# Kernel optimization log

Measured on AMD Instinct MI355X. Metric: run time of the kernel, lower is better.

Reference implementation:

```python
import jax, jax.numpy as jnp
import numpy as np

NUM_HEADS = 8

def setup_inputs() -> dict:
    key = jax.random.key(0)
    k1, k2, k3, k4, k5 = jax.random.split(key, 5)
    B, N, C = 4, 2048, 512
    x = jax.random.normal(k1, (B, N, C), dtype=jnp.float32)
    s = 1.0 / np.sqrt(C)
    qkv_w = jax.random.uniform(k2, (3 * C, C), dtype=jnp.float32, minval=-s, maxval=s)
    qkv_b = jax.random.uniform(k3, (3 * C,), dtype=jnp.float32, minval=-s, maxval=s)
    proj_w = jax.random.uniform(k4, (C, C), dtype=jnp.float32, minval=-s, maxval=s)
    proj_b = jax.random.uniform(k5, (C,), dtype=jnp.float32, minval=-s, maxval=s)
    return {"x": x, "qkv_w": qkv_w, "qkv_b": qkv_b, "proj_w": proj_w, "proj_b": proj_b}

def reference(x, qkv_w, qkv_b, proj_w, proj_b):
    B, N, C = x.shape
    H = NUM_HEADS
    D = C // H
    scale = D ** -0.5
    # qkv: [B,N,3C] -> [3,B,H,N,D]
    qkv = (jnp.einsum('bnc,oc->bno', x, qkv_w) + qkv_b)
    qkv = qkv.reshape(B, N, 3, H, D).transpose(2, 0, 3, 1, 4)
    q, k, v = qkv[0], qkv[1], qkv[2]
    attn = jnp.einsum('bhnd,bhmd->bhnm', q, k) * scale  # [B,H,N,N]
    attn = jax.nn.softmax(attn, axis=-1)
    out = jnp.einsum('bhnm,bhmd->bhnd', attn, v)  # [B,H,N,D]
    out = out.transpose(0, 2, 1, 3).reshape(B, N, C)
    return jnp.einsum('bnc,oc->bno', out, proj_w) + proj_b
```

## Files before the change

kernel.cpp:

```cpp
#include <hip/hip_runtime.h>
#include <stdint.h>


typedef short bf16x8 __attribute__((ext_vector_type(8)));
typedef float f32x2  __attribute__((ext_vector_type(2)));
typedef float f32x4  __attribute__((ext_vector_type(4)));
typedef float f32x16 __attribute__((ext_vector_type(16)));
typedef unsigned int u32x4 __attribute__((ext_vector_type(4)));

__device__ __forceinline__ unsigned short f2bf(float f) {
    unsigned int u = __builtin_bit_cast(unsigned int, f);
    u += 0x7fffu + ((u >> 16) & 1u);
    return (unsigned short)(u >> 16);
}
__device__ __forceinline__ unsigned int pk2(float a, float b) {
    return (unsigned int)f2bf(a) | ((unsigned int)f2bf(b) << 16);
}
__device__ __forceinline__ float fexp2(float x) {
    return __builtin_amdgcn_exp2f(x);
}
__device__ __forceinline__ bf16x8 ld8_f32(const float* __restrict__ p) {
    float4 f0 = *(const float4*)p;
    float4 f1 = *(const float4*)(p + 4);
    u32x4 u = {pk2(f0.x, f0.y), pk2(f0.z, f0.w), pk2(f1.x, f1.y), pk2(f1.z, f1.w)};
    return __builtin_bit_cast(bf16x8, u);
}
__device__ __forceinline__ void async16(const void* g, void* l) {
    __builtin_amdgcn_global_load_lds(
        (const __attribute__((address_space(1))) unsigned int*)g,
        (__attribute__((address_space(3))) unsigned int*)l,
        16, 0, 0);
}

#define MFMA16(a, b, c) __builtin_amdgcn_mfma_f32_16x16x32_bf16((a), (b), (c), 0, 0, 0)
#define MFMA32(a, b, c) __builtin_amdgcn_mfma_f32_32x32x16_bf16((a), (b), (c), 0, 0, 0)

__global__ void cvt_bf16(const float* __restrict__ x,
                         const float* __restrict__ w,
                         const float* __restrict__ w2,
                         unsigned short* __restrict__ xb,
                         unsigned short* __restrict__ wb,
                         unsigned short* __restrict__ wb2)
{
    const int G = 524288 + 98304 + 32768;
    for (int idx = blockIdx.x * 256 + threadIdx.x; idx < G; idx += gridDim.x * 256) {
        if (idx < 524288)
            *(bf16x8*)(xb + (size_t)idx * 8) = ld8_f32(x + (size_t)idx * 8);
        else if (idx < 524288 + 98304) {
            int j = idx - 524288;
            *(bf16x8*)(wb + (size_t)j * 8) = ld8_f32(w + (size_t)j * 8);
        } else {
            int j = idx - 524288 - 98304;
            *(bf16x8*)(wb2 + (size_t)j * 8) = ld8_f32(w2 + (size_t)j * 8);
        }
    }
}

__global__ __launch_bounds__(256, 4)
void gemm_qkv(const unsigned short* __restrict__ A,
              const unsigned short* __restrict__ B,
              const float* __restrict__ bias,
              unsigned short* __restrict__ out0,
              unsigned short* __restrict__ out1,
              unsigned short* __restrict__ out2,
              int K)
{
    __shared__ unsigned short sA[128 * 32];
    __shared__ unsigned short sB[128 * 32];

    const int tid  = threadIdx.x;
    const int wave = tid >> 6, lane = tid & 63;
    const int l = lane & 15, q16 = lane >> 4;
    const int wm = wave >> 1, wn = wave & 1;
    const int bid = blockIdx.x;
    const int slot = bid >> 3;
    const int m0 = ((bid & 7) * 8 + slot / 12) * 128;
    const int n0 = (slot % 12) * 128;

    f32x4 acc[4][4];
#pragma unroll
    for (int i = 0; i < 4; ++i)
#pragma unroll
        for (int j = 0; j < 4; ++j)
            acc[i][j] = (f32x4){0.f, 0.f, 0.f, 0.f};

    for (int k0 = 0; k0 < K; k0 += 32) {
#pragma unroll
        for (int call = 0; call < 2; ++call) {
            int L = call * 256 + tid;
            int r = L >> 2, c = L & 3;
            async16(A + (size_t)(m0 + r) * K + k0 + c * 8, sA + L * 8);
            async16(B + (size_t)(n0 + r) * K + k0 + c * 8, sB + L * 8);
        }
        __syncthreads();

        bf16x8 af[4], bfr[4];
#pragma unroll
        for (int i = 0; i < 4; ++i)
            af[i] = *(const bf16x8*)(sA + ((wm * 64 + i * 16 + l) * 4 + q16) * 8);
#pragma unroll
        for (int j = 0; j < 4; ++j)
            bfr[j] = *(const bf16x8*)(sB + ((wn * 64 + j * 16 + l) * 4 + q16) * 8);
#pragma unroll
        for (int i = 0; i < 4; ++i)
#pragma unroll
            for (int j = 0; j < 4; ++j)
                acc[i][j] = MFMA16(af[i], bfr[j], acc[i][j]);
        __syncthreads();
    }

    const float lscale = 0.18033688f;
#pragma unroll
    for (int i = 0; i < 4; ++i) {
#pragma unroll
        for (int j = 0; j < 4; ++j) {
            int col = n0 + wn * 64 + j * 16 + l;
            float bv = bias[col];
#pragma unroll
            for (int r = 0; r < 4; ++r) {
                int row = m0 + wm * 64 + i * 16 + q16 * 4 + r;
                float val = acc[i][j][r] + bv;
                int which = col >> 9;
                int h = (col >> 6) & 7, d = col & 63;
                int b = row >> 11, n = row & 2047;
                if (which == 0)
                    out0[(size_t)(((b * 8 + h) * 2048) + n) * 64 + d] = f2bf(val * lscale);
                else if (which == 1)
                    out1[(size_t)(((b * 8 + h) * 2048) + n) * 64 + d] = f2bf(val);
                else {
                    int np = (n & ~12) | ((n & 8) >> 1) | ((n & 4) << 1);
                    out2[(size_t)(((b * 8 + h) * 64) + d) * 2048 + np] = f2bf(val);
                }
            }
        }
    }
}

__global__ __launch_bounds__(256, 4)
void gemm_out(const unsigned short* __restrict__ A,
              const unsigned short* __restrict__ B,
              const float* __restrict__ bias,
              float* __restrict__ outf,
              int K, int N)
{
    __shared__ unsigned short sA[64 * 32];
    __shared__ unsigned short sB[128 * 32];

    const int tid  = threadIdx.x;
    const int wave = tid >> 6, lane = tid & 63;
    const int l = lane & 15, q16 = lane >> 4;
    const int wm = wave >> 1, wn = wave & 1;
    const int bid = blockIdx.x;
    const int slot = bid >> 3;
    const int m0 = ((bid & 7) * 16 + (slot >> 2)) * 64;
    const int n0 = (slot & 3) * 128;

    f32x4 acc[2][4];
#pragma unroll
    for (int i = 0; i < 2; ++i)
#pragma unroll
        for (int j = 0; j < 4; ++j)
            acc[i][j] = (f32x4){0.f, 0.f, 0.f, 0.f};

    for (int k0 = 0; k0 < K; k0 += 32) {
        {
            int r = tid >> 2, c = tid & 3;
            async16(A + (size_t)(m0 + r) * K + k0 + c * 8, sA + tid * 8);
        }
#pragma unroll
        for (int call = 0; call < 2; ++call) {
            int L = call * 256 + tid;
            int r = L >> 2, c = L & 3;
            async16(B + (size_t)(n0 + r) * K + k0 + c * 8, sB + L * 8);
        }
        __syncthreads();

        bf16x8 af[2], bfr[4];
#pragma unroll
        for (int i = 0; i < 2; ++i)
            af[i] = *(const bf16x8*)(sA + ((wm * 32 + i * 16 + l) * 4 + q16) * 8);
#pragma unroll
        for (int j = 0; j < 4; ++j)
            bfr[j] = *(const bf16x8*)(sB + ((wn * 64 + j * 16 + l) * 4 + q16) * 8);
#pragma unroll
        for (int i = 0; i < 2; ++i)
#pragma unroll
            for (int j = 0; j < 4; ++j)
                acc[i][j] = MFMA16(af[i], bfr[j], acc[i][j]);
        __syncthreads();
    }

#pragma unroll
    for (int i = 0; i < 2; ++i) {
#pragma unroll
        for (int j = 0; j < 4; ++j) {
            int col = n0 + wn * 64 + j * 16 + l;
            float bv = bias[col];
#pragma unroll
            for (int r = 0; r < 4; ++r) {
                int row = m0 + wm * 32 + i * 16 + q16 * 4 + r;
                outf[(size_t)row * N + col] = acc[i][j][r] + bv;
            }
        }
    }
}

__global__ __launch_bounds__(256, 2)
void attn_fused(const unsigned short* __restrict__ Q,
                const unsigned short* __restrict__ Km,
                const unsigned short* __restrict__ Vt,
                unsigned short* __restrict__ O)
{
    __shared__ unsigned short sK[2][128 * 64];
    __shared__ unsigned short sVt[2][64 * 128];

    const int tid  = threadIdx.x;
    const int wave = tid >> 6, lane = tid & 63;
    const int l31 = lane & 31, h = lane >> 5;
    const int swz = l31 & 7;
    const int bid = blockIdx.x;
    const int slot = bid >> 3;
    const int bh = (bid & 7) * 4 + (slot >> 4);
    const int n0 = (slot & 15) * 128;
    const int q0 = n0 + wave * 32;

    const unsigned short* Kp = Km + (size_t)bh * 2048 * 64;
    const unsigned short* Vp = Vt + (size_t)bh * 64 * 2048;
    const unsigned short* sKf = &sK[0][0];
    const unsigned short* sVf = &sVt[0][0];

    int ka[4], va[2][2];
#pragma unroll
    for (int ks = 0; ks < 4; ++ks)
        ka[ks] = l31 * 64 + ((ks * 2 + h) ^ swz) * 8;
#pragma unroll
    for (int m1 = 0; m1 < 2; ++m1)
#pragma unroll
        for (int ks2 = 0; ks2 < 2; ++ks2)
            va[m1][ks2] = l31 * 128 + ((m1 * 4 + ks2 * 2 + h) ^ swz) * 8;

    int ksrc[4], vsrc[4], dst[4];
#pragma unroll
    for (int c = 0; c < 4; ++c) {
        int s = wave * 256 + c * 64 + lane;
        int rk = s >> 3;
        ksrc[c] = rk * 64 + ((s & 7) ^ (rk & 7)) * 8;
        int rv = s >> 4;
        vsrc[c] = rv * 2048 + ((s & 15) ^ (rv & 7)) * 8;
        dst[c] = s * 8;
    }

    bf16x8 qf[4];
#pragma unroll
    for (int ks = 0; ks < 4; ++ks)
        qf[ks] = *(const bf16x8*)(Q + (size_t)(bh * 2048 + q0 + l31) * 64 + ks * 16 + h * 8);

    f32x16 oacc[2];
#pragma unroll
    for (int dt = 0; dt < 2; ++dt)
#pragma unroll
        for (int e = 0; e < 16; ++e) oacc[dt][e] = 0.f;
    f32x16 Zv;
#pragma unroll
    for (int e = 0; e < 16; ++e) Zv[e] = 0.f;
    f32x2 l2 = {0.f, 0.f};

#pragma unroll
    for (int c = 0; c < 4; ++c) {
        async16(Kp + ksrc[c], (void*)(sKf + dst[c]));
        async16(Vp + vsrc[c], (void*)(sVf + dst[c]));
    }
    __syncthreads();

    for (int it = 0; it < 16; ++it) {
        const int nb = ((it + 1) & 1) * 8192;
        if (it < 15) {
            int kv = (it + 1) * 128;
#pragma unroll
            for (int c = 0; c < 4; ++c)
                async16(Kp + (size_t)kv * 64 + ksrc[c], (void*)(sKf + nb + dst[c]));
        }

        f32x16 sacc[4];
#pragma unroll
        for (int mt = 0; mt < 4; ++mt) {
            bf16x8 kf0 = *(const bf16x8*)(sKf + ka[0] + mt * 2048);
            sacc[mt] = MFMA32(kf0, qf[0], Zv);
#pragma unroll
            for (int ks = 1; ks < 4; ++ks) {
                bf16x8 kf = *(const bf16x8*)(sKf + ka[ks] + mt * 2048);
                sacc[mt] = MFMA32(kf, qf[ks], sacc[mt]);
            }
        }

        if (it < 15) {
            int kv = (it + 1) * 128;
#pragma unroll
            for (int c = 0; c < 4; ++c)
                async16(Vp + (size_t)kv + vsrc[c], (void*)(sVf + nb + dst[c]));
        }

        unsigned int pk[4][4][2];
#pragma unroll
        for (int mt = 0; mt < 4; ++mt)
#pragma unroll
            for (int g = 0; g < 4; ++g) {
                float p0 = fexp2(sacc[mt][4 * g + 0]);
                float p1 = fexp2(sacc[mt][4 * g + 1]);
                float p2 = fexp2(sacc[mt][4 * g + 2]);
                float p3 = fexp2(sacc[mt][4 * g + 3]);
                l2 += (f32x2){p0, p1};
                l2 += (f32x2){p2, p3};
                pk[mt][g][0] = __builtin_amdgcn_perm(
                    __builtin_bit_cast(unsigned int, p1),
                    __builtin_bit_cast(unsigned int, p0), 0x07060302u);
                pk[mt][g][1] = __builtin_amdgcn_perm(
                    __builtin_bit_cast(unsigned int, p3),
                    __builtin_bit_cast(unsigned int, p2), 0x07060302u);
            }

#pragma unroll
        for (int mt = 0; mt < 4; ++mt) {
#pragma unroll
            for (int ks2 = 0; ks2 < 2; ++ks2) {
                u32x4 bu;
                bu[0] = pk[mt][2 * ks2][0];
                bu[1] = pk[mt][2 * ks2][1];
                bu[2] = pk[mt][2 * ks2 + 1][0];
                bu[3] = pk[mt][2 * ks2 + 1][1];
                bf16x8 bfrag = __builtin_bit_cast(bf16x8, bu);
#pragma unroll
                for (int dt = 0; dt < 2; ++dt) {
                    bf16x8 vf = *(const bf16x8*)(sVf + va[mt & 1][ks2]
                                                 + (mt >> 1) * 64 + dt * 4096);
                    oacc[dt] = MFMA32(vf, bfrag, oacc[dt]);
                }
            }
        }

#pragma unroll
        for (int ks = 0; ks < 4; ++ks) ka[ks] ^= 8192;
        va[0][0] ^= 8192; va[0][1] ^= 8192; va[1][0] ^= 8192; va[1][1] ^= 8192;
        __syncthreads();
    }

    float l_run = l2[0] + l2[1];
    l_run += __shfl_xor(l_run, 32);
    const int b = bh >> 3, hh = bh & 7;
    float inv = 1.f / fmaxf(l_run, 1e-20f);
    unsigned short* obase = O + ((size_t)(b * 2048 + q0 + l31)) * 512 + hh * 64;
#pragma unroll
    for (int dt = 0; dt < 2; ++dt)
#pragma unroll
        for (int g = 0; g < 4; ++g) {
            int d = dt * 32 + 8 * g + 4 * h;
            unsigned int w0 = pk2(oacc[dt][4 * g + 0] * inv, oacc[dt][4 * g + 1] * inv);
            unsigned int w1 = pk2(oacc[dt][4 * g + 2] * inv, oacc[dt][4 * g + 3] * inv);
            uint2 w = {w0, w1};
            *(uint2*)(obase + d) = w;
        }
}

extern "C" void kernel_launch(void* const* d_in, const int* in_sizes, int n_in,
                              void* d_out, int out_size, void* d_ws, size_t ws_size,
                              hipStream_t stream)
{
    const float* x      = (const float*)d_in[0];
    const float* qkv_w  = (const float*)d_in[1];
    const float* qkv_b  = (const float*)d_in[2];
    const float* proj_w = (const float*)d_in[3];
    const float* proj_b = (const float*)d_in[4];

    const size_t PER = 4u * 8u * 2048u * 64u;
    unsigned short* q_ws  = (unsigned short*)d_ws;
    unsigned short* k_ws  = q_ws  + PER;
    unsigned short* vt_ws = k_ws  + PER;
    unsigned short* ao_ws = vt_ws + PER;
    unsigned short* wb2   = ao_ws + PER;

    unsigned short* xb = (unsigned short*)d_out;
    unsigned short* wb = xb + PER;

    cvt_bf16<<<dim3(640), 256, 0, stream>>>(x, qkv_w, proj_w, xb, wb, wb2);
    gemm_qkv<<<dim3(768), 256, 0, stream>>>(xb, wb, qkv_b, q_ws, k_ws, vt_ws, 512);
    attn_fused<<<dim3(512), 256, 0, stream>>>(q_ws, k_ws, vt_ws, ao_ws);
    gemm_out<<<dim3(512), 256, 0, stream>>>(ao_ws, wb2, proj_b, (float*)d_out, 512, 512);
}
```

Before: 156.1 us.

## Process two query tiles per wave in attention, halving waves per block

The attention kernel now runs with 2 waves of 128 threads instead of 4, and each wave handles 64 query rows as two 32-row tiles. Each K and V fragment read from shared memory is reused across both tiles, cutting LDS reads per MFMA. Each thread issues twice as many async copies, and register pressure roughly doubles for the accumulators. Launch bounds drop to one block per SM, which lowers wave-level parallelism and may limit latency hiding.

```diff
diff --git a/kernel.cpp b/kernel.cpp
--- a/kernel.cpp
+++ b/kernel.cpp
@@ -205,7 +205,7 @@
     }
 }
 
-__global__ __launch_bounds__(256, 2)
+__global__ __launch_bounds__(128, 1)
 void attn_fused(const unsigned short* __restrict__ Q,
                 const unsigned short* __restrict__ Km,
                 const unsigned short* __restrict__ Vt,
@@ -222,7 +222,7 @@
     const int slot = bid >> 3;
     const int bh = (bid & 7) * 4 + (slot >> 4);
     const int n0 = (slot & 15) * 128;
-    const int q0 = n0 + wave * 32;
+    const int q0 = n0 + wave * 64;
 
     const unsigned short* Kp = Km + (size_t)bh * 2048 * 64;
     const unsigned short* Vp = Vt + (size_t)bh * 64 * 2048;
@@ -239,10 +239,10 @@
         for (int ks2 = 0; ks2 < 2; ++ks2)
             va[m1][ks2] = l31 * 128 + ((m1 * 4 + ks2 * 2 + h) ^ swz) * 8;
 
-    int ksrc[4], vsrc[4], dst[4];
-#pragma unroll
-    for (int c = 0; c < 4; ++c) {
-        int s = wave * 256 + c * 64 + lane;
+    int ksrc[8], vsrc[8], dst[8];
+#pragma unroll
+    for (int c = 0; c < 8; ++c) {
+        int s = c * 128 + tid;
         int rk = s >> 3;
         ksrc[c] = rk * 64 + ((s & 7) ^ (rk & 7)) * 8;
         int rv = s >> 4;
@@ -250,23 +250,30 @@
         dst[c] = s * 8;
     }
 
-    bf16x8 qf[4];
-#pragma unroll
-    for (int ks = 0; ks < 4; ++ks)
-        qf[ks] = *(const bf16x8*)(Q + (size_t)(bh * 2048 + q0 + l31) * 64 + ks * 16 + h * 8);
-
-    f32x16 oacc[2];
-#pragma unroll
-    for (int dt = 0; dt < 2; ++dt)
-#pragma unroll
-        for (int e = 0; e < 16; ++e) oacc[dt][e] = 0.f;
+    bf16x8 qf[2][4];
+#pragma unroll
+    for (int qt = 0; qt < 2; ++qt)
+#pragma unroll
+        for (int ks = 0; ks < 4; ++ks)
+            qf[qt][ks] = *(const bf16x8*)(Q + (size_t)(bh * 2048 + q0 + qt * 32 + l31) * 64
+                                          + ks * 16 + h * 8);
+
+    f32x16 oacc[2][2];
+#pragma unroll
+    for (int qt = 0; qt < 2; ++qt)
+#pragma unroll
+        for (int dt = 0; dt < 2; ++dt)
+#pragma unroll
+            for (int e = 0; e < 16; ++e) oacc[qt][dt][e] = 0.f;
     f32x16 Zv;
 #pragma unroll
     for (int e = 0; e < 16; ++e) Zv[e] = 0.f;
-    f32x2 l2 = {0.f, 0.f};
-
-#pragma unroll
-    for (int c = 0; c < 4; ++c) {
+    f32x2 l2[2];
+    l2[0] = (f32x2){0.f, 0.f};
+    l2[1] = (f32x2){0.f, 0.f};
+
+#pragma unroll
+    for (int c = 0; c < 8; ++c) {
         async16(Kp + ksrc[c], (void*)(sKf + dst[c]));
         async16(Vp + vsrc[c], (void*)(sVf + dst[c]));
     }
@@ -277,63 +284,71 @@
         if (it < 15) {
             int kv = (it + 1) * 128;
 #pragma unroll
-            for (int c = 0; c < 4; ++c)
+            for (int c = 0; c < 8; ++c)
                 async16(Kp + (size_t)kv * 64 + ksrc[c], (void*)(sKf + nb + dst[c]));
         }
 
-        f32x16 sacc[4];
+        f32x16 sacc[2][4];
 #pragma unroll
         for (int mt = 0; mt < 4; ++mt) {
             bf16x8 kf0 = *(const bf16x8*)(sKf + ka[0] + mt * 2048);
-            sacc[mt] = MFMA32(kf0, qf[0], Zv);
+            sacc[0][mt] = MFMA32(kf0, qf[0][0], Zv);
+            sacc[1][mt] = MFMA32(kf0, qf[1][0], Zv);
 #pragma unroll
             for (int ks = 1; ks < 4; ++ks) {
                 bf16x8 kf = *(const bf16x8*)(sKf + ka[ks] + mt * 2048);
-                sacc[mt] = MFMA32(kf, qf[ks], sacc[mt]);
+                sacc[0][mt] = MFMA32(kf, qf[0][ks], sacc[0][mt]);
+                sacc[1][mt] = MFMA32(kf, qf[1][ks], sacc[1][mt]);
             }
         }
 
         if (it < 15) {
             int kv = (it + 1) * 128;
 #pragma unroll
-            for (int c = 0; c < 4; ++c)
+            for (int c = 0; c < 8; ++c)
                 async16(Vp + (size_t)kv + vsrc[c], (void*)(sVf + nb + dst[c]));
         }
 
-        unsigned int pk[4][4][2];
-#pragma unroll
-        for (int mt = 0; mt < 4; ++mt)
-#pragma unroll
-            for (int g = 0; g < 4; ++g) {
-                float p0 = fexp2(sacc[mt][4 * g + 0]);
-                float p1 = fexp2(sacc[mt][4 * g + 1]);
-                float p2 = fexp2(sacc[mt][4 * g + 2]);
-                float p3 = fexp2(sacc[mt][4 * g + 3]);
-                l2 += (f32x2){p0, p1};
-                l2 += (f32x2){p2, p3};
-                pk[mt][g][0] = __builtin_amdgcn_perm(
-                    __builtin_bit_cast(unsigned int, p1),
-                    __builtin_bit_cast(unsigned int, p0), 0x07060302u);
-                pk[mt][g][1] = __builtin_amdgcn_perm(
-                    __builtin_bit_cast(unsigned int, p3),
-                    __builtin_bit_cast(unsigned int, p2), 0x07060302u);
-            }
-
 #pragma unroll
         for (int mt = 0; mt < 4; ++mt) {
+            unsigned int pk[2][4][2];
+#pragma unroll
+            for (int qt = 0; qt < 2; ++qt) {
+#pragma unroll
+                for (int g = 0; g < 4; ++g) {
+                    float p0 = fexp2(sacc[qt][mt][4 * g + 0]);
+                    float p1 = fexp2(sacc[qt][mt][4 * g + 1]);
+                    float p2 = fexp2(sacc[qt][mt][4 * g + 2]);
+                    float p3 = fexp2(sacc[qt][mt][4 * g + 3]);
+                    l2[qt] += (f32x2){p0, p1};
+                    l2[qt] += (f32x2){p2, p3};
+                    pk[qt][g][0] = __builtin_amdgcn_perm(
+                        __builtin_bit_cast(unsigned int, p1),
+                        __builtin_bit_cast(unsigned int, p0), 0x07060302u);
+                    pk[qt][g][1] = __builtin_amdgcn_perm(
+                        __builtin_bit_cast(unsigned int, p3),
+                        __builtin_bit_cast(unsigned int, p2), 0x07060302u);
+                }
+            }
 #pragma unroll
             for (int ks2 = 0; ks2 < 2; ++ks2) {
-                u32x4 bu;
-                bu[0] = pk[mt][2 * ks2][0];
-                bu[1] = pk[mt][2 * ks2][1];
-                bu[2] = pk[mt][2 * ks2 + 1][0];
-                bu[3] = pk[mt][2 * ks2 + 1][1];
-                bf16x8 bfrag = __builtin_bit_cast(bf16x8, bu);
+                u32x4 bu0, bu1;
+                bu0[0] = pk[0][2 * ks2][0];
+                bu0[1] = pk[0][2 * ks2][1];
+                bu0[2] = pk[0][2 * ks2 + 1][0];
+                bu0[3] = pk[0][2 * ks2 + 1][1];
+                bu1[0] = pk[1][2 * ks2][0];
+                bu1[1] = pk[1][2 * ks2][1];
+                bu1[2] = pk[1][2 * ks2 + 1][0];
+                bu1[3] = pk[1][2 * ks2 + 1][1];
+                bf16x8 bf0 = __builtin_bit_cast(bf16x8, bu0);
+                bf16x8 bf1 = __builtin_bit_cast(bf16x8, bu1);
 #pragma unroll
                 for (int dt = 0; dt < 2; ++dt) {
                     bf16x8 vf = *(const bf16x8*)(sVf + va[mt & 1][ks2]
                                                  + (mt >> 1) * 64 + dt * 4096);
-                    oacc[dt] = MFMA32(vf, bfrag, oacc[dt]);
+                    oacc[0][dt] = MFMA32(vf, bf0, oacc[0][dt]);
+                    oacc[1][dt] = MFMA32(vf, bf1, oacc[1][dt]);
                 }
             }
         }
@@ -344,21 +359,26 @@
         __syncthreads();
     }
 
-    float l_run = l2[0] + l2[1];
-    l_run += __shfl_xor(l_run, 32);
     const int b = bh >> 3, hh = bh & 7;
-    float inv = 1.f / fmaxf(l_run, 1e-20f);
-    unsigned short* obase = O + ((size_t)(b * 2048 + q0 + l31)) * 512 + hh * 64;
-#pragma unroll
-    for (int dt = 0; dt < 2; ++dt)
-#pragma unroll
-        for (int g = 0; g < 4; ++g) {
-            int d = dt * 32 + 8 * g + 4 * h;
-            unsigned int w0 = pk2(oacc[dt][4 * g + 0] * inv, oacc[dt][4 * g + 1] * inv);
-            unsigned int w1 = pk2(oacc[dt][4 * g + 2] * inv, oacc[dt][4 * g + 3] * inv);
-            uint2 w = {w0, w1};
-            *(uint2*)(obase + d) = w;
-        }
+#pragma unroll
+    for (int qt = 0; qt < 2; ++qt) {
+        float l_run = l2[qt][0] + l2[qt][1];
+        l_run += __shfl_xor(l_run, 32);
+        float inv = 1.f / fmaxf(l_run, 1e-20f);
+        unsigned short* obase = O + ((size_t)(b * 2048 + q0 + qt * 32 + l31)) * 512 + hh * 64;
+#pragma unroll
+        for (int dt = 0; dt < 2; ++dt)
+#pragma unroll
+            for (int g = 0; g < 4; ++g) {
+                int d = dt * 32 + 8 * g + 4 * h;
+                unsigned int w0 = pk2(oacc[qt][dt][4 * g + 0] * inv,
+                                      oacc[qt][dt][4 * g + 1] * inv);
+                unsigned int w1 = pk2(oacc[qt][dt][4 * g + 2] * inv,
+                                      oacc[qt][dt][4 * g + 3] * inv);
+                uint2 w = {w0, w1};
+                *(uint2*)(obase + d) = w;
+            }
+    }
 }
 
 extern "C" void kernel_launch(void* const* d_in, const int* in_sizes, int n_in,
@@ -383,6 +403,6 @@
 
     cvt_bf16<<<dim3(640), 256, 0, stream>>>(x, qkv_w, proj_w, xb, wb, wb2);
     gemm_qkv<<<dim3(768), 256, 0, stream>>>(xb, wb, qkv_b, q_ws, k_ws, vt_ws, 512);
-    attn_fused<<<dim3(512), 256, 0, stream>>>(q_ws, k_ws, vt_ws, ao_ws);
+    attn_fused<<<dim3(512), 128, 0, stream>>>(q_ws, k_ws, vt_ws, ao_ws);
     gemm_out<<<dim3(512), 256, 0, stream>>>(ao_ws, wb2, proj_b, (float*)d_out, 512, 512);
 }
```

After: 169.9 us. 1.09x slower.

## Split attention KV tiles across wave pairs and reduce partial outputs in LDS

Applied to the files above, without the earlier changes.

The attention kernel now runs 512 threads per block. Each pair of waves shares 32 query rows and splits every 128-wide KV tile, so each wave handles 64 keys. At the end, partial O accumulators and row sums from the second wave of each pair are added through shared memory before normalization. This halves per-wave MFMA work and register pressure (pk array shrinks) to raise occupancy and latency hiding. The cost is an extra LDS reduction with a block-wide sync and half the waves idle during the epilogue.

```diff
diff --git a/kernel.cpp b/kernel.cpp
--- a/kernel.cpp
+++ b/kernel.cpp
@@ -205,55 +205,56 @@
     }
 }
 
-__global__ __launch_bounds__(256, 2)
+__global__ __launch_bounds__(512, 4)
 void attn_fused(const unsigned short* __restrict__ Q,
                 const unsigned short* __restrict__ Km,
                 const unsigned short* __restrict__ Vt,
                 unsigned short* __restrict__ O)
 {
-    __shared__ unsigned short sK[2][128 * 64];
-    __shared__ unsigned short sVt[2][64 * 128];
+    __shared__ unsigned short sAll[32768];
 
     const int tid  = threadIdx.x;
     const int wave = tid >> 6, lane = tid & 63;
     const int l31 = lane & 31, h = lane >> 5;
     const int swz = l31 & 7;
+    const int qq = wave >> 1, kh = wave & 1;
     const int bid = blockIdx.x;
     const int slot = bid >> 3;
     const int bh = (bid & 7) * 4 + (slot >> 4);
     const int n0 = (slot & 15) * 128;
-    const int q0 = n0 + wave * 32;
+    const int q0 = n0 + qq * 32;
 
     const unsigned short* Kp = Km + (size_t)bh * 2048 * 64;
     const unsigned short* Vp = Vt + (size_t)bh * 64 * 2048;
-    const unsigned short* sKf = &sK[0][0];
-    const unsigned short* sVf = &sVt[0][0];
+    unsigned short* sKf = sAll;
+    unsigned short* sVf = sAll + 16384;
 
     int ka[4], va[2][2];
 #pragma unroll
     for (int ks = 0; ks < 4; ++ks)
-        ka[ks] = l31 * 64 + ((ks * 2 + h) ^ swz) * 8;
+        ka[ks] = (kh * 64 + l31) * 64 + ((ks * 2 + h) ^ swz) * 8;
 #pragma unroll
     for (int m1 = 0; m1 < 2; ++m1)
 #pragma unroll
         for (int ks2 = 0; ks2 < 2; ++ks2)
-            va[m1][ks2] = l31 * 128 + ((m1 * 4 + ks2 * 2 + h) ^ swz) * 8;
-
-    int ksrc[4], vsrc[4], dst[4];
-#pragma unroll
-    for (int c = 0; c < 4; ++c) {
-        int s = wave * 256 + c * 64 + lane;
+            va[m1][ks2] = l31 * 128 + ((m1 * 4 + ks2 * 2 + h) ^ swz) * 8 + kh * 64;
+
+    int ksrc[2], vsrc[2], dstv[2];
+#pragma unroll
+    for (int c = 0; c < 2; ++c) {
+        int s = c * 512 + tid;
         int rk = s >> 3;
         ksrc[c] = rk * 64 + ((s & 7) ^ (rk & 7)) * 8;
         int rv = s >> 4;
         vsrc[c] = rv * 2048 + ((s & 15) ^ (rv & 7)) * 8;
-        dst[c] = s * 8;
+        dstv[c] = s * 8;
     }
 
     bf16x8 qf[4];
 #pragma unroll
     for (int ks = 0; ks < 4; ++ks)
-        qf[ks] = *(const bf16x8*)(Q + (size_t)(bh * 2048 + q0 + l31) * 64 + ks * 16 + h * 8);
+        qf[ks] = *(const bf16x8*)(Q + (size_t)(bh * 2048 + q0 + l31) * 64
+                                  + ks * 16 + h * 8);
 
     f32x16 oacc[2];
 #pragma unroll
@@ -266,9 +267,9 @@
     f32x2 l2 = {0.f, 0.f};
 
 #pragma unroll
-    for (int c = 0; c < 4; ++c) {
-        async16(Kp + ksrc[c], (void*)(sKf + dst[c]));
-        async16(Vp + vsrc[c], (void*)(sVf + dst[c]));
+    for (int c = 0; c < 2; ++c) {
+        async16(Kp + ksrc[c], (void*)(sKf + dstv[c]));
+        async16(Vp + vsrc[c], (void*)(sVf + dstv[c]));
     }
     __syncthreads();
 
@@ -277,13 +278,13 @@
         if (it < 15) {
             int kv = (it + 1) * 128;
 #pragma unroll
-            for (int c = 0; c < 4; ++c)
-                async16(Kp + (size_t)kv * 64 + ksrc[c], (void*)(sKf + nb + dst[c]));
-        }
-
-        f32x16 sacc[4];
-#pragma unroll
-        for (int mt = 0; mt < 4; ++mt) {
+            for (int c = 0; c < 2; ++c)
+                async16(Kp + (size_t)kv * 64 + ksrc[c], (void*)(sKf + nb + dstv[c]));
+        }
+
+        f32x16 sacc[2];
+#pragma unroll
+        for (int mt = 0; mt < 2; ++mt) {
             bf16x8 kf0 = *(const bf16x8*)(sKf + ka[0] + mt * 2048);
             sacc[mt] = MFMA32(kf0, qf[0], Zv);
 #pragma unroll
@@ -296,13 +297,13 @@
         if (it < 15) {
             int kv = (it + 1) * 128;
 #pragma unroll
-            for (int c = 0; c < 4; ++c)
-                async16(Vp + (size_t)kv + vsrc[c], (void*)(sVf + nb + dst[c]));
-        }
-
-        unsigned int pk[4][4][2];
-#pragma unroll
-        for (int mt = 0; mt < 4; ++mt)
+            for (int c = 0; c < 2; ++c)
+                async16(Vp + (size_t)kv + vsrc[c], (void*)(sVf + nb + dstv[c]));
+        }
+
+#pragma unroll
+        for (int mt = 0; mt < 2; ++mt) {
+            unsigned int pk[4][2];
 #pragma unroll
             for (int g = 0; g < 4; ++g) {
                 float p0 = fexp2(sacc[mt][4 * g + 0]);
@@ -311,28 +312,24 @@
                 float p3 = fexp2(sacc[mt][4 * g + 3]);
                 l2 += (f32x2){p0, p1};
                 l2 += (f32x2){p2, p3};
-                pk[mt][g][0] = __builtin_amdgcn_perm(
+                pk[g][0] = __builtin_amdgcn_perm(
                     __builtin_bit_cast(unsigned int, p1),
                     __builtin_bit_cast(unsigned int, p0), 0x07060302u);
-                pk[mt][g][1] = __builtin_amdgcn_perm(
+                pk[g][1] = __builtin_amdgcn_perm(
                     __builtin_bit_cast(unsigned int, p3),
                     __builtin_bit_cast(unsigned int, p2), 0x07060302u);
             }
-
-#pragma unroll
-        for (int mt = 0; mt < 4; ++mt) {
 #pragma unroll
             for (int ks2 = 0; ks2 < 2; ++ks2) {
                 u32x4 bu;
-                bu[0] = pk[mt][2 * ks2][0];
-                bu[1] = pk[mt][2 * ks2][1];
-                bu[2] = pk[mt][2 * ks2 + 1][0];
-                bu[3] = pk[mt][2 * ks2 + 1][1];
+                bu[0] = pk[2 * ks2][0];
+                bu[1] = pk[2 * ks2][1];
+                bu[2] = pk[2 * ks2 + 1][0];
+                bu[3] = pk[2 * ks2 + 1][1];
                 bf16x8 bfrag = __builtin_bit_cast(bf16x8, bu);
 #pragma unroll
                 for (int dt = 0; dt < 2; ++dt) {
-                    bf16x8 vf = *(const bf16x8*)(sVf + va[mt & 1][ks2]
-                                                 + (mt >> 1) * 64 + dt * 4096);
+                    bf16x8 vf = *(const bf16x8*)(sVf + va[mt][ks2] + dt * 4096);
                     oacc[dt] = MFMA32(vf, bfrag, oacc[dt]);
                 }
             }
@@ -344,21 +341,47 @@
         __syncthreads();
     }
 
-    float l_run = l2[0] + l2[1];
-    l_run += __shfl_xor(l_run, 32);
-    const int b = bh >> 3, hh = bh & 7;
-    float inv = 1.f / fmaxf(l_run, 1e-20f);
-    unsigned short* obase = O + ((size_t)(b * 2048 + q0 + l31)) * 512 + hh * 64;
-#pragma unroll
-    for (int dt = 0; dt < 2; ++dt)
-#pragma unroll
-        for (int g = 0; g < 4; ++g) {
-            int d = dt * 32 + 8 * g + 4 * h;
-            unsigned int w0 = pk2(oacc[dt][4 * g + 0] * inv, oacc[dt][4 * g + 1] * inv);
-            unsigned int w1 = pk2(oacc[dt][4 * g + 2] * inv, oacc[dt][4 * g + 3] * inv);
-            uint2 w = {w0, w1};
-            *(uint2*)(obase + d) = w;
-        }
+    float* sf = (float*)sAll;
+    float* sl = sf + 8192;
+    if (kh == 1) {
+        const int base = qq * 2048 + lane * 32;
+#pragma unroll
+        for (int dt = 0; dt < 2; ++dt) {
+            int chunk = dt ^ (lane & 1);
+            *(f32x16*)(sf + base + chunk * 16) = oacc[dt];
+        }
+        *(f32x2*)(sl + qq * 128 + lane * 2) = l2;
+    }
+    __syncthreads();
+    if (kh == 0) {
+        const int base = qq * 2048 + lane * 32;
+#pragma unroll
+        for (int dt = 0; dt < 2; ++dt) {
+            int chunk = dt ^ (lane & 1);
+            f32x16 part = *(const f32x16*)(sf + base + chunk * 16);
+#pragma unroll
+            for (int e = 0; e < 16; ++e) oacc[dt][e] += part[e];
+        }
+        l2 += *(const f32x2*)(sl + qq * 128 + lane * 2);
+
+        float l_run = l2[0] + l2[1];
+        l_run += __shfl_xor(l_run, 32);
+        float inv = 1.f / fmaxf(l_run, 1e-20f);
+        const int b = bh >> 3, hh = bh & 7;
+        unsigned short* obase = O + ((size_t)(b * 2048 + q0 + l31)) * 512 + hh * 64;
+#pragma unroll
+        for (int dt = 0; dt < 2; ++dt)
+#pragma unroll
+            for (int g = 0; g < 4; ++g) {
+                int d = dt * 32 + 8 * g + 4 * h;
+                unsigned int w0 = pk2(oacc[dt][4 * g + 0] * inv,
+                                      oacc[dt][4 * g + 1] * inv);
+                unsigned int w1 = pk2(oacc[dt][4 * g + 2] * inv,
+                                      oacc[dt][4 * g + 3] * inv);
+                uint2 w = {w0, w1};
+                *(uint2*)(obase + d) = w;
+            }
+    }
 }
 
 extern "C" void kernel_launch(void* const* d_in, const int* in_sizes, int n_in,
@@ -383,6 +406,6 @@
 
     cvt_bf16<<<dim3(640), 256, 0, stream>>>(x, qkv_w, proj_w, xb, wb, wb2);
     gemm_qkv<<<dim3(768), 256, 0, stream>>>(xb, wb, qkv_b, q_ws, k_ws, vt_ws, 512);
-    attn_fused<<<dim3(512), 256, 0, stream>>>(q_ws, k_ws, vt_ws, ao_ws);
+    attn_fused<<<dim3(512), 512, 0, stream>>>(q_ws, k_ws, vt_ws, ao_ws);
     gemm_out<<<dim3(512), 256, 0, stream>>>(ao_ws, wb2, proj_b, (float*)d_out, 512, 512);
 }
```

Result: no change. 158.6 us (+1.6%).
